# Performance work log

Hardware: AMD Instinct MI355X
Metric: run time of the kernel (lower is better)

## Reference

```python
import jax, jax.numpy as jnp
import numpy as np

N, E, B, L = 32768, 524288, 64, 512  # nodes, edges, graphs, max nodes/graph
V, D, H = 10000, 256, 512            # vocab, embed_dim, hidden_dim


def gcn_conv(h, W, b, src, dst, n):
    """PyG GCNConv: add self-loops, symmetric deg normalization, scatter-sum."""
    h = h @ W  # [n, out]
    loops = jnp.arange(n)
    s = jnp.concatenate([src, loops])
    d = jnp.concatenate([dst, loops])
    deg = jax.ops.segment_sum(jnp.ones_like(d, dtype=h.dtype), d, num_segments=n)
    dinv = jnp.where(deg > 0, jax.lax.rsqrt(deg), 0.0)
    norm = dinv[s] * dinv[d]  # [E+n]
    out = jax.ops.segment_sum(h[s] * norm[:, None], d, num_segments=n)
    return out + b


def gru_seq(x, Wih, Whh, bih, bhh):
    """torch nn.GRU (1 layer, batch_first). x: [B, T, H] -> outputs [T, B, H]."""
    def step(h, x_t):
        gi = x_t @ Wih.T + bih          # [B, 3H]
        gh = h @ Whh.T + bhh            # [B, 3H]
        ir, iz, inn = jnp.split(gi, 3, axis=-1)
        hr, hz, hn = jnp.split(gh, 3, axis=-1)
        r = jax.nn.sigmoid(ir + hr)
        z = jax.nn.sigmoid(iz + hz)
        n = jnp.tanh(inn + r * hn)
        h = (1.0 - z) * n + z * h
        return h, h
    h0 = jnp.zeros((x.shape[0], Whh.shape[1]), x.dtype)
    _, outs = jax.lax.scan(step, h0, jnp.swapaxes(x, 0, 1))
    return outs  # [T, B, H]


def setup_inputs() -> dict:
    key = jax.random.key(0)
    ks = jax.random.split(key, 16)
    s = 0.05
    x = jax.random.randint(ks[0], (N,), 0, V)
    edge_index = jax.random.randint(ks[1], (2, E), 0, N)
    batch_idx = jnp.arange(N) // L  # sorted graph ids, L nodes per graph
    focal_points = jax.random.uniform(ks[2], (B, 1), jnp.float32)
    return {
        "x": x, "edge_index": edge_index, "batch_idx": batch_idx,
        "focal_points": focal_points,
        "emb": jax.random.normal(ks[3], (V, D), jnp.float32) * s,
        "W1": jax.random.normal(ks[4], (D, H), jnp.float32) * s,
        "b1": jnp.zeros((H,), jnp.float32),
        "W2": jax.random.normal(ks[5], (H, H), jnp.float32) * s,
        "b2": jnp.zeros((H,), jnp.float32),
        "Wih": jax.random.normal(ks[6], (3 * H, H), jnp.float32) * s,
        "Whh": jax.random.normal(ks[7], (3 * H, H), jnp.float32) * s,
        "bih": jnp.zeros((3 * H,), jnp.float32),
        "bhh": jnp.zeros((3 * H,), jnp.float32),
        "fc1_w": jax.random.normal(ks[8], (H + 1, H), jnp.float32) * s,
        "fc1_b": jnp.zeros((H,), jnp.float32),
        "fc2_w": jax.random.normal(ks[9], (H, 1), jnp.float32) * s,
        "fc2_b": jnp.zeros((1,), jnp.float32),
    }


def reference(x, edge_index, batch_idx, focal_points, emb, W1, b1, W2, b2,
              Wih, Whh, bih, bhh, fc1_w, fc1_b, fc2_w, fc2_b):
    src, dst = edge_index[0], edge_index[1]
    h = emb[x]  # [N, D]
    h = jax.nn.relu(gcn_conv(h, W1, b1, src, dst, N))
    h = jax.nn.relu(gcn_conv(h, W2, b2, src, dst, N))  # [N, H]

    # Ragged -> padded: scatter each node to (graph, position-within-graph)
    ones = jnp.ones((N,), h.dtype)
    counts = jax.ops.segment_sum(ones, batch_idx, num_segments=B)
    starts = jnp.cumsum(counts) - counts  # exclusive cumsum
    pos = jnp.arange(N) - starts[batch_idx].astype(jnp.int32)
    padded = jnp.zeros((B, L, H), h.dtype).at[batch_idx, pos].set(h)

    gru_out = gru_seq(padded, Wih, Whh, bih, bhh)   # [L, B, H]
    graph_emb = gru_out.mean(axis=0)                # [B, H]
    g = jnp.concatenate([graph_emb, focal_points], axis=1)  # [B, H+1]
    out = jax.nn.relu(g @ fc1_w + fc1_b)
    out = jax.nn.sigmoid(out @ fc2_w + fc2_b)       # [B, 1]
    return out
```

## Files before the change

kernel.cpp:

```cpp
#include <hip/hip_runtime.h>

#define NODES 32768
#define EDGES 524288
#define BGR   64
#define LSEQ  512
#define DEMB  256
#define HDIM  512

typedef unsigned short u16;
typedef unsigned int   u32;
typedef unsigned long long u64;
typedef __attribute__((ext_vector_type(8))) short short8;
typedef __attribute__((ext_vector_type(4))) float f32x4;

__device__ __forceinline__ float bf2f(u16 u){ u32 x = ((u32)u)<<16; float f; __builtin_memcpy(&f,&x,4); return f; }
__device__ __forceinline__ u16 f2bf(float f){ u32 x; __builtin_memcpy(&x,&f,4); u32 r = x + 0x7fffu + ((x>>16)&1u); return (u16)(r>>16); }
__device__ __forceinline__ float lo16(u32 u){ u32 x = u<<16; float f; __builtin_memcpy(&f,&x,4); return f; }
__device__ __forceinline__ float hi16(u32 u){ u32 x = u & 0xffff0000u; float f; __builtin_memcpy(&f,&x,4); return f; }
__device__ __forceinline__ u32 pack2(float a, float b){ return (u32)f2bf(a) | ((u32)f2bf(b)<<16); }


__global__ void zero_i32(int* p, int n){
  int i = blockIdx.x*256 + threadIdx.x;
  if (i < n) p[i] = 0;
}

__global__ void transpose_cast(const float* __restrict__ in, u16* __restrict__ out, int K, int N){
  int i = blockIdx.x*256 + threadIdx.x;
  if (i < N*K){ int n = i / K, k = i - n*K; out[i] = f2bf(in[(size_t)k*N + n]); }
}

__global__ void cast_bf(const float* __restrict__ in, u16* __restrict__ out, int n){
  int i = blockIdx.x*256 + threadIdx.x;
  if (i < n) out[i] = f2bf(in[i]);
}

__global__ void count_indeg(const int* __restrict__ dst, int* __restrict__ indeg){
  int e = blockIdx.x*256 + threadIdx.x;
  if (e < EDGES) atomicAdd(&indeg[dst[e]], 1);
}

__global__ void compute_dinv(const int* __restrict__ indeg, float* __restrict__ dinv){
  int i = blockIdx.x*256 + threadIdx.x;
  if (i < NODES) dinv[i] = rsqrtf((float)(indeg[i] + 1));
}

__global__ __launch_bounds__(1024) void scan_csr(const int* __restrict__ indeg,
                                                 int* __restrict__ row_ptr,
                                                 int* __restrict__ cursor){
  __shared__ int part[1024];
  int tid = threadIdx.x, base = tid*32;
  int loc[32]; int s = 0;
  for (int i=0;i<32;i++){ loc[i] = s; s += indeg[base+i]; }
  part[tid] = s; __syncthreads();
  for (int off=1; off<1024; off<<=1){
    int v = part[tid]; int add = (tid>=off) ? part[tid-off] : 0;
    __syncthreads(); part[tid] = v + add; __syncthreads();
  }
  int offt = (tid==0) ? 0 : part[tid-1];
  for (int i=0;i<32;i++){ int v = offt + loc[i]; row_ptr[base+i] = v; cursor[base+i] = v; }
}

__global__ void fill_csr(const int* __restrict__ src, const int* __restrict__ dst,
                         int* __restrict__ cursor, int* __restrict__ csr_src){
  int e = blockIdx.x*256 + threadIdx.x;
  if (e < EDGES){ int d = dst[e]; int p = atomicAdd(&cursor[d], 1); csr_src[p] = src[e]; }
}

__global__ __launch_bounds__(256) void agg_emb(const int* __restrict__ x, const float* __restrict__ emb,
    const float* __restrict__ dinv, const int* __restrict__ row_ptr, const int* __restrict__ indeg,
    const int* __restrict__ csr_src, u16* __restrict__ out){
  int node = blockIdx.x*4 + (threadIdx.x>>6);
  int lane = threadIdx.x & 63;
  float di = dinv[node];
  int xi = x[node];
  f32x4 acc = ((const f32x4*)(emb + (size_t)xi*DEMB))[lane] * di;
  int st = row_ptr[node], cn = indeg[node];
  for (int p = st; p < st+cn; p++){
    int s = csr_src[p];
    float ws = dinv[s];
    int xs = x[s];
    acc += ((const f32x4*)(emb + (size_t)xs*DEMB))[lane] * ws;
  }
  acc *= di;
  u64 pv = (u64)pack2(acc[0],acc[1]) | ((u64)pack2(acc[2],acc[3])<<32);
  *(u64*)(out + (size_t)node*DEMB + lane*4) = pv;
}

__global__ __launch_bounds__(256) void agg_h(const u16* __restrict__ hin, const float* __restrict__ dinv,
    const int* __restrict__ row_ptr, const int* __restrict__ indeg,
    const int* __restrict__ csr_src, u16* __restrict__ out){
  int node = blockIdx.x*4 + (threadIdx.x>>6);
  int lane = threadIdx.x & 63;
  float di = dinv[node];
  float a[8];
  uint4 hv = *((const uint4*)(hin + (size_t)node*HDIM) + lane);
  a[0]=lo16(hv.x)*di; a[1]=hi16(hv.x)*di; a[2]=lo16(hv.y)*di; a[3]=hi16(hv.y)*di;
  a[4]=lo16(hv.z)*di; a[5]=hi16(hv.z)*di; a[6]=lo16(hv.w)*di; a[7]=hi16(hv.w)*di;
  int st = row_ptr[node], cn = indeg[node];
  for (int p = st; p < st+cn; p++){
    int s = csr_src[p];
    float ws = dinv[s];
    uint4 v = *((const uint4*)(hin + (size_t)s*HDIM) + lane);
    a[0]+=lo16(v.x)*ws; a[1]+=hi16(v.x)*ws; a[2]+=lo16(v.y)*ws; a[3]+=hi16(v.y)*ws;
    a[4]+=lo16(v.z)*ws; a[5]+=hi16(v.z)*ws; a[6]+=lo16(v.w)*ws; a[7]+=hi16(v.w)*ws;
  }
  uint4 o; o.x=pack2(a[0]*di,a[1]*di); o.y=pack2(a[2]*di,a[3]*di);
  o.z=pack2(a[4]*di,a[5]*di); o.w=pack2(a[6]*di,a[7]*di);
  *(uint4*)(out + (size_t)node*HDIM + lane*8) = o;
}

#define BM 128
#define BN 128
#define BKK 32
__global__ __launch_bounds__(256) void gemm_bt(const u16* __restrict__ A, const u16* __restrict__ BT,
    const float* __restrict__ bias, u16* __restrict__ C, int M, int N, int K, int relu){
  __shared__ u16 aS[BM][BKK+8];
  __shared__ u16 bS[BN][BKK+8];
  int tid = threadIdx.x;
  int m0 = blockIdx.y * BM, n0 = blockIdx.x * BN;
  int lane = tid & 63, w = tid >> 6;
  int wm = w >> 1, wn = w & 1;
  f32x4 acc[4][4];
  for (int i=0;i<4;i++) for (int j=0;j<4;j++) acc[i][j] = (f32x4)0.0f;

  int r  = tid >> 1;
  int cc = (tid & 1) * 16;
  const u16* Ag = A + (size_t)(m0 + r) * K + cc;
  const u16* Bg = BT + (size_t)(n0 + r) * K + cc;
  int l15 = lane & 15, q8 = (lane >> 4) * 8;

  for (int k0 = 0; k0 < K; k0 += BKK) {
    uint4 av0 = *(const uint4*)(Ag + k0);
    uint4 av1 = *(const uint4*)(Ag + k0 + 8);
    uint4 bv0 = *(const uint4*)(Bg + k0);
    uint4 bv1 = *(const uint4*)(Bg + k0 + 8);
    *(uint4*)&aS[r][cc]   = av0; *(uint4*)&aS[r][cc+8] = av1;
    *(uint4*)&bS[r][cc]   = bv0; *(uint4*)&bS[r][cc+8] = bv1;
    __syncthreads();
    short8 af[4], bfr[4];
    for (int i=0;i<4;i++) af[i]  = *(const short8*)&aS[wm*64 + i*16 + l15][q8];
    for (int j=0;j<4;j++) bfr[j] = *(const short8*)&bS[wn*64 + j*16 + l15][q8];
    for (int i=0;i<4;i++)
      for (int j=0;j<4;j++)
        acc[i][j] = __builtin_amdgcn_mfma_f32_16x16x32_bf16(af[i], bfr[j], acc[i][j], 0, 0, 0);
    __syncthreads();
  }
  int q = lane >> 4;
  for (int i=0;i<4;i++) for (int j=0;j<4;j++){
    int col = n0 + wn*64 + j*16 + l15;
    float bval = bias[col];
    for (int rr=0; rr<4; rr++){
      int row = m0 + wm*64 + i*16 + q*4 + rr;
      float v = acc[i][j][rr] + bval;
      if (relu) v = fmaxf(v, 0.f);
      C[(size_t)row * N + col] = f2bf(v);
    }
  }
}

__global__ __launch_bounds__(512) void gru_kernel(const u16* __restrict__ gi,
    const float* __restrict__ Whh, const float* __restrict__ bhh,
    float* __restrict__ graph_emb, u16* __restrict__ xbuf, int* __restrict__ cnt){
  __shared__ u16  w_lds[96*520];
  __shared__ u16  h_lds[16*520];
  __shared__ float gh_lds[16*100];

  int tid = threadIdx.x;
  int g = blockIdx.x >> 4, j = blockIdx.x & 15;
  int lane = tid & 63, wave = tid >> 6;

  for (int idx = tid; idx < 96*512; idx += 512){
    int rr = idx >> 9, c = idx & 511;
    int grow = (rr >> 5) * 512 + j*32 + (rr & 31);
    w_lds[rr*520 + c] = f2bf(Whh[(size_t)grow*512 + c]);
  }
  for (int idx = tid; idx < 16*520; idx += 512) h_lds[idx] = 0;

  int b = tid >> 5, hh = tid & 31;
  int bg = g*16 + b;
  int c_r = j*32 + hh, c_z = 512 + j*32 + hh, c_n = 1024 + j*32 + hh;
  float bias_r = bhh[c_r], bias_z = bhh[c_z], bias_n = bhh[c_n];
  const u16* gi_row = gi + (size_t)bg * LSEQ * 1536;
  float h_prev = 0.f, accm = 0.f;
  int l15 = lane & 15, q8 = (lane>>4)*8, qr = (lane>>4)*4;

  u32* xbuf32 = (u32*)xbuf;

  int ro0 = ((tid       ) >> 7)*520 + ((tid       ) & 127)*4;
  int ro1 = ((tid +  512) >> 7)*520 + ((tid +  512) & 127)*4;
  int ro2 = ((tid + 1024) >> 7)*520 + ((tid + 1024) & 127)*4;
  int ro3 = ((tid + 1536) >> 7)*520 + ((tid + 1536) & 127)*4;

  u16 g_r = gi_row[c_r], g_z = gi_row[c_z], g_n = gi_row[c_n];

  __syncthreads();

  for (int t = 0; t < LSEQ; t++){
    if (wave < 6){
      f32x4 acc0 = (f32x4)0.0f, acc1 = (f32x4)0.0f;
      const u16* wrow = &w_lds[(wave*16 + l15)*520];
      const u16* hrow = &h_lds[l15*520];
      #pragma unroll
      for (int k0 = 0; k0 < 256; k0 += 32){
        acc0 = __builtin_amdgcn_mfma_f32_16x16x32_bf16(*(const short8*)(hrow + k0 + q8),
                                                       *(const short8*)(wrow + k0 + q8), acc0, 0, 0, 0);
        acc1 = __builtin_amdgcn_mfma_f32_16x16x32_bf16(*(const short8*)(hrow + 256 + k0 + q8),
                                                       *(const short8*)(wrow + 256 + k0 + q8), acc1, 0, 0, 0);
      }
      f32x4 acc = acc0 + acc1;
      int col = wave*16 + l15;
      #pragma unroll
      for (int rr2 = 0; rr2 < 4; rr2++) gh_lds[(qr + rr2)*100 + col] = acc[rr2];
    }
    __syncthreads();

    float ghr = gh_lds[b*100 + hh]      + bias_r;
    float ghz = gh_lds[b*100 + 32 + hh] + bias_z;
    float ghn = gh_lds[b*100 + 64 + hh] + bias_n;
    float rg = 1.f / (1.f + __expf(-(bf2f(g_r) + ghr)));
    float zg = 1.f / (1.f + __expf(-(bf2f(g_z) + ghz)));
    float pre = bf2f(g_n) + rg * ghn;
    pre = fminf(fmaxf(pre, -20.f), 20.f);
    float e2 = __expf(2.f * pre);
    float nn = (e2 - 1.f) / (e2 + 1.f);
    float h_new = (1.f - zg) * nn + zg * h_prev;
    accm += h_new; h_prev = h_new;

    float h_nb = __shfl_xor(h_new, 1, 64);
    if ((hh & 1) == 0){
      u32 pv = pack2(h_new, h_nb);
      u32* dst32 = xbuf32 + ((size_t)(g*2 + (t&1))*16 + b)*256 + ((j*32 + hh) >> 1);
      __hip_atomic_store(dst32, pv, __ATOMIC_RELAXED, __HIP_MEMORY_SCOPE_AGENT);
    }
    asm volatile("s_waitcnt vmcnt(0)" ::: "memory");

    int tn = (t + 1 < LSEQ) ? t + 1 : t;
    const u16* gp = gi_row + (size_t)tn * 1536;
    u16 n_r = gp[c_r], n_z = gp[c_z], n_n = gp[c_n];

    __syncthreads();
    if (tid == 0){
      __hip_atomic_fetch_add(&cnt[g], 1, __ATOMIC_RELAXED, __HIP_MEMORY_SCOPE_AGENT);
      int target = 16*(t+1);
      while (__hip_atomic_load(&cnt[g], __ATOMIC_RELAXED, __HIP_MEMORY_SCOPE_AGENT) < target)
        __builtin_amdgcn_s_sleep(1);
    }
    __syncthreads();

    u64* src = (u64*)(xbuf + (size_t)(g*2 + (t&1))*16*512);
    u64 r0 = __hip_atomic_load(src + tid,        __ATOMIC_RELAXED, __HIP_MEMORY_SCOPE_AGENT);
    u64 r1 = __hip_atomic_load(src + tid +  512, __ATOMIC_RELAXED, __HIP_MEMORY_SCOPE_AGENT);
    u64 r2 = __hip_atomic_load(src + tid + 1024, __ATOMIC_RELAXED, __HIP_MEMORY_SCOPE_AGENT);
    u64 r3 = __hip_atomic_load(src + tid + 1536, __ATOMIC_RELAXED, __HIP_MEMORY_SCOPE_AGENT);
    *(u64*)&h_lds[ro0] = r0;
    *(u64*)&h_lds[ro1] = r1;
    *(u64*)&h_lds[ro2] = r2;
    *(u64*)&h_lds[ro3] = r3;
    __syncthreads();

    g_r = n_r; g_z = n_z; g_n = n_n;
  }
  graph_emb[(size_t)bg*512 + j*32 + hh] = accm * (1.f/512.f);
}

__global__ __launch_bounds__(256) void head(const float* __restrict__ graph_emb, const float* __restrict__ focal,
    const float* __restrict__ fc1w, const float* __restrict__ fc1b,
    const float* __restrict__ fc2w, const float* __restrict__ fc2b, float* __restrict__ out){
  __shared__ float gv[513];
  __shared__ float h1s[512];
  __shared__ float red[4];
  int bq = blockIdx.x, tid = threadIdx.x;
  for (int i = tid; i < 512; i += 256) gv[i] = graph_emb[(size_t)bq*512 + i];
  if (tid == 0) gv[512] = focal[bq];
  __syncthreads();
  for (int c = tid; c < 512; c += 256){
    float acc = fc1b[c];
    for (int k = 0; k < 513; k++) acc += gv[k] * fc1w[(size_t)k*512 + c];
    h1s[c] = fmaxf(acc, 0.f);
  }
  __syncthreads();
  float p = h1s[tid]*fc2w[tid] + h1s[tid+256]*fc2w[tid+256];
  for (int off = 32; off; off >>= 1) p += __shfl_down(p, off, 64);
  if ((tid & 63) == 0) red[tid >> 6] = p;
  __syncthreads();
  if (tid == 0){
    float s = red[0]+red[1]+red[2]+red[3] + fc2b[0];
    out[bq] = 1.f / (1.f + __expf(-s));
  }
}

extern "C" void kernel_launch(void* const* d_in, const int* in_sizes, int n_in,
                              void* d_out, int out_size, void* d_ws, size_t ws_size,
                              hipStream_t stream){
  const int*   x     = (const int*)d_in[0];
  const int*   edge  = (const int*)d_in[1];
  const int*   srcp  = edge;
  const int*   dstp  = edge + EDGES;
  const float* focal = (const float*)d_in[3];
  const float* emb   = (const float*)d_in[4];
  const float* W1    = (const float*)d_in[5];
  const float* b1    = (const float*)d_in[6];
  const float* W2    = (const float*)d_in[7];
  const float* b2    = (const float*)d_in[8];
  const float* Wih   = (const float*)d_in[9];
  const float* Whh   = (const float*)d_in[10];
  const float* bih   = (const float*)d_in[11];
  const float* bhh   = (const float*)d_in[12];
  const float* fc1w  = (const float*)d_in[13];
  const float* fc1b  = (const float*)d_in[14];
  const float* fc2w  = (const float*)d_in[15];
  const float* fc2b  = (const float*)d_in[16];

  char* ws = (char*)d_ws;
  constexpr size_t H2_OFF    = 0;
  constexpr size_t AGG1_OFF  = 33554432;
  constexpr size_t H1_OFF    = 50331648;
  constexpr size_t AGG2_OFF  = 83886080;
  constexpr size_t GI_OFF    = 33554432;
  constexpr size_t MISC      = 134217728;
  constexpr size_t INDEG_OFF = MISC;
  constexpr size_t CNT_OFF   = MISC + 131072;
  constexpr size_t DINV_OFF  = MISC + 131328;
  constexpr size_t ROWPTR_OFF= MISC + 262400;
  constexpr size_t CURSOR_OFF= MISC + 393472;
  constexpr size_t CSR_OFF   = MISC + 524544;
  constexpr size_t W1T_OFF   = MISC + 2621696;
  constexpr size_t W2T_OFF   = MISC + 2883840;
  constexpr size_t WIHB_OFF  = MISC + 3408128;
  constexpr size_t XBUF_OFF  = MISC + 4980992;
  constexpr size_t GEMB_OFF  = MISC + 5112064;

  int*   indeg  = (int*)(ws + INDEG_OFF);
  int*   cntp   = (int*)(ws + CNT_OFF);
  float* dinv   = (float*)(ws + DINV_OFF);
  int*   rowptr = (int*)(ws + ROWPTR_OFF);
  int*   cursor = (int*)(ws + CURSOR_OFF);
  int*   csrsrc = (int*)(ws + CSR_OFF);
  u16*   W1T    = (u16*)(ws + W1T_OFF);
  u16*   W2T    = (u16*)(ws + W2T_OFF);
  u16*   WihB   = (u16*)(ws + WIHB_OFF);
  u16*   agg1   = (u16*)(ws + AGG1_OFF);
  u16*   h1     = (u16*)(ws + H1_OFF);
  u16*   agg2   = (u16*)(ws + AGG2_OFF);
  u16*   h2     = (u16*)(ws + H2_OFF);
  u16*   gi     = (u16*)(ws + GI_OFF);
  u16*   xbuf   = (u16*)(ws + XBUF_OFF);
  float* gemb   = (float*)(ws + GEMB_OFF);

  zero_i32<<<129, 256, 0, stream>>>(indeg, 32768 + 64);
  transpose_cast<<<512, 256, 0, stream>>>(W1, W1T, 256, 512);
  transpose_cast<<<1024, 256, 0, stream>>>(W2, W2T, 512, 512);
  cast_bf<<<3072, 256, 0, stream>>>(Wih, WihB, 1536*512);
  count_indeg<<<2048, 256, 0, stream>>>(dstp, indeg);
  compute_dinv<<<128, 256, 0, stream>>>(indeg, dinv);
  scan_csr<<<1, 1024, 0, stream>>>(indeg, rowptr, cursor);
  fill_csr<<<2048, 256, 0, stream>>>(srcp, dstp, cursor, csrsrc);
  agg_emb<<<8192, 256, 0, stream>>>(x, emb, dinv, rowptr, indeg, csrsrc, agg1);
  gemm_bt<<<dim3(4, 256), 256, 0, stream>>>(agg1, W1T, b1, h1, NODES, 512, 256, 1);
  agg_h<<<8192, 256, 0, stream>>>(h1, dinv, rowptr, indeg, csrsrc, agg2);
  gemm_bt<<<dim3(4, 256), 256, 0, stream>>>(agg2, W2T, b2, h2, NODES, 512, 512, 1);
  gemm_bt<<<dim3(12, 256), 256, 0, stream>>>(h2, WihB, bih, gi, NODES, 1536, 512, 0);
  gru_kernel<<<64, 512, 0, stream>>>(gi, Whh, bhh, gemb, xbuf, cntp);
  head<<<64, 256, 0, stream>>>(gemb, focal, fc1w, fc1b, fc2w, fc2b, (float*)d_out);
}
```

Measured before the change: 2.743 ms.

## Replace GRU counter barrier with tagged-value flags and use bf16 embedding table

The GRU's cross-block step synchronisation no longer uses an atomic counter with a spin loop on one thread plus two block barriers. Each published hidden-state word now carries a step tag in its upper 32 bits, and each reader thread polls its own 8 words until every tag matches, so readiness travels with the data. Separately, the embedding table is cast to bf16 once so agg_emb gathers half the bytes per neighbour. The tagged scheme doubles xbuf traffic and makes every thread spin, and the added cast kernel costs an extra pass over the table.

Measured after the change: 2.587 ms. 1.06x faster.

```diff
diff --git a/kernel.cpp b/kernel.cpp
--- a/kernel.cpp
+++ b/kernel.cpp
@@ -67,23 +67,25 @@
   if (e < EDGES){ int d = dst[e]; int p = atomicAdd(&cursor[d], 1); csr_src[p] = src[e]; }
 }
 
-__global__ __launch_bounds__(256) void agg_emb(const int* __restrict__ x, const float* __restrict__ emb,
+__global__ __launch_bounds__(256) void agg_emb(const int* __restrict__ x, const u16* __restrict__ embb,
     const float* __restrict__ dinv, const int* __restrict__ row_ptr, const int* __restrict__ indeg,
     const int* __restrict__ csr_src, u16* __restrict__ out){
   int node = blockIdx.x*4 + (threadIdx.x>>6);
   int lane = threadIdx.x & 63;
   float di = dinv[node];
   int xi = x[node];
-  f32x4 acc = ((const f32x4*)(emb + (size_t)xi*DEMB))[lane] * di;
+  u64 hv = *(const u64*)(embb + (size_t)xi*DEMB + lane*4);
+  u32 h0 = (u32)hv, h1 = (u32)(hv>>32);
+  float a0 = lo16(h0)*di, a1 = hi16(h0)*di, a2 = lo16(h1)*di, a3 = hi16(h1)*di;
   int st = row_ptr[node], cn = indeg[node];
   for (int p = st; p < st+cn; p++){
     int s = csr_src[p];
     float ws = dinv[s];
-    int xs = x[s];
-    acc += ((const f32x4*)(emb + (size_t)xs*DEMB))[lane] * ws;
-  }
-  acc *= di;
-  u64 pv = (u64)pack2(acc[0],acc[1]) | ((u64)pack2(acc[2],acc[3])<<32);
+    u64 v = *(const u64*)(embb + (size_t)x[s]*DEMB + lane*4);
+    u32 w0 = (u32)v, w1 = (u32)(v>>32);
+    a0 += lo16(w0)*ws; a1 += hi16(w0)*ws; a2 += lo16(w1)*ws; a3 += hi16(w1)*ws;
+  }
+  u64 pv = (u64)pack2(a0*di,a1*di) | ((u64)pack2(a2*di,a3*di)<<32);
   *(u64*)(out + (size_t)node*DEMB + lane*4) = pv;
 }
 
@@ -161,7 +163,7 @@
 
 __global__ __launch_bounds__(512) void gru_kernel(const u16* __restrict__ gi,
     const float* __restrict__ Whh, const float* __restrict__ bhh,
-    float* __restrict__ graph_emb, u16* __restrict__ xbuf, int* __restrict__ cnt){
+    float* __restrict__ graph_emb, u64* __restrict__ xbuf){
   __shared__ u16  w_lds[96*520];
   __shared__ u16  h_lds[16*520];
   __shared__ float gh_lds[16*100];
@@ -185,13 +187,7 @@
   float h_prev = 0.f, accm = 0.f;
   int l15 = lane & 15, q8 = (lane>>4)*8, qr = (lane>>4)*4;
 
-  u32* xbuf32 = (u32*)xbuf;
-
-  int ro0 = ((tid       ) >> 7)*520 + ((tid       ) & 127)*4;
-  int ro1 = ((tid +  512) >> 7)*520 + ((tid +  512) & 127)*4;
-  int ro2 = ((tid + 1024) >> 7)*520 + ((tid + 1024) & 127)*4;
-  int ro3 = ((tid + 1536) >> 7)*520 + ((tid + 1536) & 127)*4;
-
+  u64* xb = xbuf + (size_t)g * 8192;
   u16 g_r = gi_row[c_r], g_z = gi_row[c_z], g_n = gi_row[c_n];
 
   __syncthreads();
@@ -227,36 +223,32 @@
     float h_new = (1.f - zg) * nn + zg * h_prev;
     accm += h_new; h_prev = h_new;
 
+    u32 tag = (u32)(t + 1);
     float h_nb = __shfl_xor(h_new, 1, 64);
     if ((hh & 1) == 0){
-      u32 pv = pack2(h_new, h_nb);
-      u32* dst32 = xbuf32 + ((size_t)(g*2 + (t&1))*16 + b)*256 + ((j*32 + hh) >> 1);
-      __hip_atomic_store(dst32, pv, __ATOMIC_RELAXED, __HIP_MEMORY_SCOPE_AGENT);
+      u64 val = ((u64)tag << 32) | (u64)pack2(h_new, h_nb);
+      __hip_atomic_store(xb + (size_t)((t&1)*16 + b)*256 + j*16 + (hh>>1), val,
+                         __ATOMIC_RELAXED, __HIP_MEMORY_SCOPE_AGENT);
     }
-    asm volatile("s_waitcnt vmcnt(0)" ::: "memory");
 
     int tn = (t + 1 < LSEQ) ? t + 1 : t;
-    const u16* gp = gi_row + (size_t)tn * 1536;
-    u16 n_r = gp[c_r], n_z = gp[c_z], n_n = gp[c_n];
-
-    __syncthreads();
-    if (tid == 0){
-      __hip_atomic_fetch_add(&cnt[g], 1, __ATOMIC_RELAXED, __HIP_MEMORY_SCOPE_AGENT);
-      int target = 16*(t+1);
-      while (__hip_atomic_load(&cnt[g], __ATOMIC_RELAXED, __HIP_MEMORY_SCOPE_AGENT) < target)
-        __builtin_amdgcn_s_sleep(1);
-    }
-    __syncthreads();
-
-    u64* src = (u64*)(xbuf + (size_t)(g*2 + (t&1))*16*512);
-    u64 r0 = __hip_atomic_load(src + tid,        __ATOMIC_RELAXED, __HIP_MEMORY_SCOPE_AGENT);
-    u64 r1 = __hip_atomic_load(src + tid +  512, __ATOMIC_RELAXED, __HIP_MEMORY_SCOPE_AGENT);
-    u64 r2 = __hip_atomic_load(src + tid + 1024, __ATOMIC_RELAXED, __HIP_MEMORY_SCOPE_AGENT);
-    u64 r3 = __hip_atomic_load(src + tid + 1536, __ATOMIC_RELAXED, __HIP_MEMORY_SCOPE_AGENT);
-    *(u64*)&h_lds[ro0] = r0;
-    *(u64*)&h_lds[ro1] = r1;
-    *(u64*)&h_lds[ro2] = r2;
-    *(u64*)&h_lds[ro3] = r3;
+    const u16* gp2 = gi_row + (size_t)tn * 1536;
+    u16 n_r = gp2[c_r], n_z = gp2[c_z], n_n = gp2[c_n];
+
+    const u64* rp = xb + (size_t)((t&1)*16 + b)*256 + hh*8;
+    u64 v[8];
+    bool ok;
+    do {
+      #pragma unroll
+      for (int i=0;i<8;i++) v[i] = __hip_atomic_load(rp + i, __ATOMIC_RELAXED, __HIP_MEMORY_SCOPE_AGENT);
+      ok = true;
+      #pragma unroll
+      for (int i=0;i<8;i++) ok = ok && ((u32)(v[i] >> 32) == tag);
+    } while (!ok);
+
+    u32* hl = (u32*)h_lds + b*260 + hh*8;
+    #pragma unroll
+    for (int i=0;i<8;i++) hl[i] = (u32)v[i];
     __syncthreads();
 
     g_r = n_r; g_z = n_z; g_n = n_n;
@@ -329,10 +321,9 @@
   constexpr size_t W2T_OFF   = MISC + 2883840;
   constexpr size_t WIHB_OFF  = MISC + 3408128;
   constexpr size_t XBUF_OFF  = MISC + 4980992;
-  constexpr size_t GEMB_OFF  = MISC + 5112064;
+  constexpr size_t GEMB_OFF  = MISC + 5243136;
 
   int*   indeg  = (int*)(ws + INDEG_OFF);
-  int*   cntp   = (int*)(ws + CNT_OFF);
   float* dinv   = (float*)(ws + DINV_OFF);
   int*   rowptr = (int*)(ws + ROWPTR_OFF);
   int*   cursor = (int*)(ws + CURSOR_OFF);
@@ -343,24 +334,26 @@
   u16*   agg1   = (u16*)(ws + AGG1_OFF);
   u16*   h1     = (u16*)(ws + H1_OFF);
   u16*   agg2   = (u16*)(ws + AGG2_OFF);
+  u16*   embb   = (u16*)(ws + AGG2_OFF);
   u16*   h2     = (u16*)(ws + H2_OFF);
   u16*   gi     = (u16*)(ws + GI_OFF);
-  u16*   xbuf   = (u16*)(ws + XBUF_OFF);
+  u64*   xbuf   = (u64*)(ws + XBUF_OFF);
   float* gemb   = (float*)(ws + GEMB_OFF);
 
   zero_i32<<<129, 256, 0, stream>>>(indeg, 32768 + 64);
   transpose_cast<<<512, 256, 0, stream>>>(W1, W1T, 256, 512);
   transpose_cast<<<1024, 256, 0, stream>>>(W2, W2T, 512, 512);
   cast_bf<<<3072, 256, 0, stream>>>(Wih, WihB, 1536*512);
+  cast_bf<<<10000, 256, 0, stream>>>(emb, embb, 10000*256);
   count_indeg<<<2048, 256, 0, stream>>>(dstp, indeg);
   compute_dinv<<<128, 256, 0, stream>>>(indeg, dinv);
   scan_csr<<<1, 1024, 0, stream>>>(indeg, rowptr, cursor);
   fill_csr<<<2048, 256, 0, stream>>>(srcp, dstp, cursor, csrsrc);
-  agg_emb<<<8192, 256, 0, stream>>>(x, emb, dinv, rowptr, indeg, csrsrc, agg1);
+  agg_emb<<<8192, 256, 0, stream>>>(x, embb, dinv, rowptr, indeg, csrsrc, agg1);
   gemm_bt<<<dim3(4, 256), 256, 0, stream>>>(agg1, W1T, b1, h1, NODES, 512, 256, 1);
   agg_h<<<8192, 256, 0, stream>>>(h1, dinv, rowptr, indeg, csrsrc, agg2);
   gemm_bt<<<dim3(4, 256), 256, 0, stream>>>(agg2, W2T, b2, h2, NODES, 512, 512, 1);
   gemm_bt<<<dim3(12, 256), 256, 0, stream>>>(h2, WihB, bih, gi, NODES, 1536, 512, 0);
-  gru_kernel<<<64, 512, 0, stream>>>(gi, Whh, bhh, gemb, xbuf, cntp);
+  gru_kernel<<<64, 512, 0, stream>>>(gi, Whh, bhh, gemb, xbuf);
   head<<<64, 256, 0, stream>>>(gemb, focal, fc1w, fc1b, fc2w, fc2b, (float*)d_out);
 }
```
